# Performance work log

Hardware: AMD Instinct MI355X
Metric: run time of the kernel (lower is better)

Reference implementation:

```python
import jax, jax.numpy as jnp
import numpy as np

B, T, D = 2, 2048, 1024
H = 16
HD = D // H  # 64

def setup_inputs() -> dict:
    key = jax.random.key(0)
    k1, k2, k3 = jax.random.split(key, 3)
    x = jax.random.normal(k1, (B, T, D), dtype=jnp.float32)
    # Linear weights stored as [in, out] for x @ W (torch stores [out, in])
    W_qkv = jax.random.normal(k2, (D, 3 * D), dtype=jnp.float32) * (1.0 / np.sqrt(D))
    W_proj = jax.random.normal(k3, (D, D), dtype=jnp.float32) * (1.0 / np.sqrt(D))
    return {"x": x, "W_qkv": W_qkv, "W_proj": W_proj}

def reference(x, W_qkv, W_proj):
    Bx, Tx, C = x.shape
    qkv = x @ W_qkv                             # [B, T, 3D]
    q, k, v = jnp.split(qkv, 3, axis=-1)        # each [B, T, D]
    # [B, T, H, HD] -> [B, H, T, HD]
    q = q.reshape(Bx, Tx, H, HD).transpose(0, 2, 1, 3)
    k = k.reshape(Bx, Tx, H, HD).transpose(0, 2, 1, 3)
    v = v.reshape(Bx, Tx, H, HD).transpose(0, 2, 1, 3)
    scale = 1.0 / np.sqrt(HD).astype(np.float32)
    att = jnp.einsum('bhqd,bhkd->bhqk', q, k) * scale  # [B, H, T, T]
    causal = jnp.tril(jnp.ones((Tx, Tx), dtype=bool))
    att = jnp.where(causal[None, None, :, :], att, -jnp.inf)
    att = jax.nn.softmax(att, axis=-1)
    y = jnp.einsum('bhqk,bhkd->bhqd', att, v)   # [B, H, T, HD]
    y = y.transpose(0, 2, 1, 3).reshape(Bx, Tx, C)
    return y @ W_proj
```

## Files before the change

### kernel.cpp

```cpp
#include <hip/hip_runtime.h>

typedef __bf16 bf16x8 __attribute__((ext_vector_type(8)));
typedef __bf16 bf16x4 __attribute__((ext_vector_type(4)));
typedef float f32x4 __attribute__((ext_vector_type(4)));
typedef unsigned short u16;
typedef unsigned int u32;
typedef u32 u32x4 __attribute__((ext_vector_type(4)));

__device__ __forceinline__ u16 f2bf(float f) {
  u32 u = __builtin_bit_cast(u32, f);
  u += 0x7fffu + ((u >> 16) & 1u);
  return (u16)(u >> 16);
}

__device__ __forceinline__ u32 cvt_pk_bf16(float lo, float hi) {
  u32 r;
  asm("v_cvt_pk_bf16_f32 %0, %1, %2" : "=v"(r) : "v"(lo), "v"(hi));
  return r;
}

__device__ __forceinline__ float ex2(float x) {
  float r;
  asm("v_exp_f32 %0, %1" : "=v"(r) : "v"(x));
  return r;
}

__device__ __forceinline__ void gl_lds16(const u16* g, u16* l) {
  __builtin_amdgcn_global_load_lds(
      (const __attribute__((address_space(1))) u32*)g,
      (__attribute__((address_space(3))) u32*)l, 16, 0, 0);
}

__device__ __forceinline__ bf16x4 tr16(const u16* p) {
  bf16x4 r;
  auto lp = (const __attribute__((address_space(3))) u16*)p;
  asm volatile("ds_read_b64_tr_b16 %0, %1" : "=&v"(r) : "v"(lp));
  return r;
}

__global__ __launch_bounds__(256) void k_prep(const float* __restrict__ x,
                                              u16* __restrict__ Xb,
                                              const float* __restrict__ Wqkv,
                                              u16* __restrict__ Wqt,
                                              const float* __restrict__ Wproj,
                                              u16* __restrict__ Wpt) {
  __shared__ float tile[32][33];
  const int bid = blockIdx.x;
  if (bid < 2048) {
    int i = bid * 256 + threadIdx.x;
    const float4* p = (const float4*)x + (size_t)i * 2;
    float4 a = p[0], b = p[1];
    u16 r[8] = {f2bf(a.x), f2bf(a.y), f2bf(a.z), f2bf(a.w),
                f2bf(b.x), f2bf(b.y), f2bf(b.z), f2bf(b.w)};
    ((uint4*)Xb)[i] = *(const uint4*)r;
    return;
  }
  const float* in;
  u16* out;
  int K, N, n0, k0;
  if (bid < 5120) {
    in = Wqkv;
    out = Wqt;
    K = 1024;
    N = 3072;
    int idx = bid - 2048;
    n0 = (idx % 96) * 32;
    k0 = (idx / 96) * 32;
  } else {
    in = Wproj;
    out = Wpt;
    K = 1024;
    N = 1024;
    int idx = bid - 5120;
    n0 = (idx & 31) * 32;
    k0 = (idx >> 5) * 32;
  }
  int c = threadIdx.x & 31, r0 = (threadIdx.x >> 5) * 4;
#pragma unroll
  for (int rr = 0; rr < 4; ++rr) {
    int r = r0 + rr;
    tile[r][c] = in[(size_t)(k0 + r) * N + n0 + c];
  }
  __syncthreads();
#pragma unroll
  for (int rr = 0; rr < 4; ++rr) {
    int r = r0 + rr;
    out[(size_t)(n0 + r) * K + k0 + c] = f2bf(tile[c][r]);
  }
}

__global__ __launch_bounds__(256) void k_gemm0(const u16* __restrict__ A,
                                               const u16* __restrict__ Bt,
                                               u16* __restrict__ Qp, u16* __restrict__ Kp,
                                               u16* __restrict__ Vp, int K) {
  __shared__ char smem[128 * 136 * 2];
  u16* As = (u16*)smem;
  u16* Bs = (u16*)(smem + 16384);
  u16* Cs = (u16*)smem;
  const int tid = threadIdx.x;
  const int lane = tid & 63, wave = tid >> 6;
  const int l15 = lane & 15, l4 = lane >> 4;
  const int wr = wave >> 1, wc = wave & 1;
  const int tm = blockIdx.y, tn = blockIdx.x;

  int srow[4], scol[4];
#pragma unroll
  for (int i = 0; i < 4; ++i) {
    srow[i] = wave * 32 + i * 8 + (lane >> 3);
    scol[i] = ((lane & 7) ^ (srow[i] & 7)) * 8;
  }

  const f32x4 fz = {0.f, 0.f, 0.f, 0.f};
  f32x4 acc[4][4];
#pragma unroll
  for (int a = 0; a < 4; ++a)
#pragma unroll
    for (int b = 0; b < 4; ++b) acc[a][b] = fz;

  const int nk = K >> 6;
  for (int kt = 0; kt < nk; ++kt) {
#pragma unroll
    for (int i = 0; i < 4; ++i)
      gl_lds16(A + (size_t)(tm * 128 + srow[i]) * K + kt * 64 + scol[i],
               &As[(wave * 4 + i) * 512]);
#pragma unroll
    for (int i = 0; i < 4; ++i)
      gl_lds16(Bt + (size_t)(tn * 128 + srow[i]) * K + kt * 64 + scol[i],
               &Bs[(wave * 4 + i) * 512]);
    __syncthreads();
    bf16x8 af[2][4], bfr[2][4];
#pragma unroll
    for (int s = 0; s < 2; ++s) {
#pragma unroll
      for (int mi = 0; mi < 4; ++mi) {
        int row = wr * 64 + mi * 16 + l15;
        int pch = (s * 4 + l4) ^ (row & 7);
        af[s][mi] = *(const bf16x8*)&As[row * 64 + pch * 8];
      }
#pragma unroll
      for (int ni = 0; ni < 4; ++ni) {
        int row = wc * 64 + ni * 16 + l15;
        int pch = (s * 4 + l4) ^ (row & 7);
        bfr[s][ni] = *(const bf16x8*)&Bs[row * 64 + pch * 8];
      }
    }
    __builtin_amdgcn_s_setprio(1);
#pragma unroll
    for (int s = 0; s < 2; ++s)
#pragma unroll
      for (int mi = 0; mi < 4; ++mi)
#pragma unroll
        for (int ni = 0; ni < 4; ++ni)
          acc[mi][ni] = __builtin_amdgcn_mfma_f32_16x16x32_bf16(af[s][mi], bfr[s][ni],
                                                                acc[mi][ni], 0, 0, 0);
    __builtin_amdgcn_s_setprio(0);
    __syncthreads();
  }

#pragma unroll
  for (int ni = 0; ni < 4; ++ni) {
    int colb = wc * 64 + ni * 16;
    float scl = ((tn * 128 + colb) >> 10) == 0 ? 0.180336880f : 1.0f;
#pragma unroll
    for (int mi = 0; mi < 4; ++mi)
#pragma unroll
      for (int r = 0; r < 4; ++r) {
        int rowb = wr * 64 + mi * 16 + l4 * 4 + r;
        Cs[rowb * 136 + colb + l15] = f2bf(acc[mi][ni][r] * scl);
      }
  }
  __syncthreads();
#pragma unroll
  for (int pass = 0; pass < 8; ++pass) {
    int rowb = pass * 16 + (tid >> 4);
    int colb = (tid & 15) * 8;
    uint4 v = *(const uint4*)&Cs[rowb * 136 + colb];
    int rowg = tm * 128 + rowb;
    int b = rowg >> 11, t = rowg & 2047;
    int gcol = tn * 128 + colb;
    int which = gcol >> 10;
    int d = gcol & 1023;
    int h = d >> 6, hd = d & 63;
    u16* dst = which == 0 ? Qp : (which == 1 ? Kp : Vp);
    *(uint4*)&dst[(size_t)(((b * 16 + h) * 2048 + t) * 64 + hd)] = v;
  }
}

__global__ __launch_bounds__(256) void k_gemm1(const u16* __restrict__ A,
                                               const u16* __restrict__ Bt,
                                               float* __restrict__ Cf, int K) {
  __shared__ char smem1[128 * 68 * 4];
  u16* As = (u16*)smem1;
  u16* Bs = (u16*)(smem1 + 16384);
  float* Cs = (float*)smem1;
  const int tid = threadIdx.x;
  const int lane = tid & 63, wave = tid >> 6;
  const int l15 = lane & 15, l4 = lane >> 4;
  const int wr = wave >> 1, wc = wave & 1;
  const int tm = blockIdx.y, tn = blockIdx.x;

  int srowA[4], scolA[4], srowB[2], scolB[2];
#pragma unroll
  for (int i = 0; i < 4; ++i) {
    srowA[i] = wave * 32 + i * 8 + (lane >> 3);
    scolA[i] = ((lane & 7) ^ (srowA[i] & 7)) * 8;
  }
#pragma unroll
  for (int i = 0; i < 2; ++i) {
    srowB[i] = wave * 16 + i * 8 + (lane >> 3);
    scolB[i] = ((lane & 7) ^ (srowB[i] & 7)) * 8;
  }

  const f32x4 fz = {0.f, 0.f, 0.f, 0.f};
  f32x4 acc[4][2];
#pragma unroll
  for (int a = 0; a < 4; ++a)
#pragma unroll
    for (int b = 0; b < 2; ++b) acc[a][b] = fz;

  const int nk = K >> 6;
  for (int kt = 0; kt < nk; ++kt) {
#pragma unroll
    for (int i = 0; i < 4; ++i)
      gl_lds16(A + (size_t)(tm * 128 + srowA[i]) * K + kt * 64 + scolA[i],
               &As[(wave * 4 + i) * 512]);
#pragma unroll
    for (int i = 0; i < 2; ++i)
      gl_lds16(Bt + (size_t)(tn * 64 + srowB[i]) * K + kt * 64 + scolB[i],
               &Bs[(wave * 2 + i) * 512]);
    __syncthreads();
    bf16x8 af[2][4], bfr[2][2];
#pragma unroll
    for (int s = 0; s < 2; ++s) {
#pragma unroll
      for (int mi = 0; mi < 4; ++mi) {
        int row = wr * 64 + mi * 16 + l15;
        int pch = (s * 4 + l4) ^ (row & 7);
        af[s][mi] = *(const bf16x8*)&As[row * 64 + pch * 8];
      }
#pragma unroll
      for (int ni = 0; ni < 2; ++ni) {
        int row = wc * 32 + ni * 16 + l15;
        int pch = (s * 4 + l4) ^ (row & 7);
        bfr[s][ni] = *(const bf16x8*)&Bs[row * 64 + pch * 8];
      }
    }
    __builtin_amdgcn_s_setprio(1);
#pragma unroll
    for (int s = 0; s < 2; ++s)
#pragma unroll
      for (int mi = 0; mi < 4; ++mi)
#pragma unroll
        for (int ni = 0; ni < 2; ++ni)
          acc[mi][ni] = __builtin_amdgcn_mfma_f32_16x16x32_bf16(af[s][mi], bfr[s][ni],
                                                                acc[mi][ni], 0, 0, 0);
    __builtin_amdgcn_s_setprio(0);
    __syncthreads();
  }

#pragma unroll
  for (int mi = 0; mi < 4; ++mi)
#pragma unroll
    for (int ni = 0; ni < 2; ++ni)
#pragma unroll
      for (int r = 0; r < 4; ++r) {
        int rowb = wr * 64 + mi * 16 + l4 * 4 + r;
        Cs[rowb * 68 + wc * 32 + ni * 16 + l15] = acc[mi][ni][r];
      }
  __syncthreads();
#pragma unroll
  for (int pass = 0; pass < 8; ++pass) {
    int rowb = pass * 16 + (tid >> 4);
    int colb = (tid & 15) * 4;
    float4 v = *(const float4*)&Cs[rowb * 68 + colb];
    *(float4*)&Cf[(size_t)(tm * 128 + rowb) * 1024 + tn * 64 + colb] = v;
  }
}

__global__ __launch_bounds__(256) void k_attn(const u16* __restrict__ Q,
                                              const u16* __restrict__ K,
                                              const u16* __restrict__ V,
                                              u16* __restrict__ Y) {
  __shared__ u16 Kl[4][64 * 64];
  __shared__ u16 Vtr[4][64 * 64];
  const int tid = threadIdx.x, lane = tid & 63, wave = tid >> 6;
  const int l15 = lane & 15, l4 = lane >> 4;
  const int L = blockIdx.y * 16 + blockIdx.x;
  const int g = L & 7, j = L >> 3;
  const int bh = (g << 2) + (j >> 4);
  const int pp = j & 15;
  const int qtA = 31 - pp, qtB = pp;
  const u16* Qb = Q + (size_t)bh * 2048 * 64;
  const u16* Kb = K + (size_t)bh * 2048 * 64;
  const u16* Vb = V + (size_t)bh * 2048 * 64;
  const int b = bh >> 4, h = bh & 15;
  const f32x4 fz = {0.f, 0.f, 0.f, 0.f};

  const int kk0 = wave * 16 + (lane >> 3);
  const int kk1 = kk0 + 8;
  const int lcol0 = ((lane & 7) ^ (kk0 & 7)) * 8;
  const int lcol1 = ((lane & 7) ^ (kk1 & 7)) * 8;
  int vk[2], vhd[2];
#pragma unroll
  for (int i = 0; i < 2; ++i) {
    int o = (wave * 2 + i) * 512 + lane * 8;
    vk[i] = ((o >> 6) & 15) * 4 + ((o >> 4) & 3);
    vhd[i] = ((o >> 10) << 4) + (o & 8);
  }

  auto stage = [&](int buf, int kt) {
    gl_lds16(Kb + (size_t)(kt * 64 + kk0) * 64 + lcol0, &Kl[buf][(wave * 2 + 0) * 512]);
    gl_lds16(Kb + (size_t)(kt * 64 + kk1) * 64 + lcol1, &Kl[buf][(wave * 2 + 1) * 512]);
    gl_lds16(Vb + (size_t)(kt * 64 + vk[0]) * 64 + vhd[0], &Vtr[buf][(wave * 2 + 0) * 512]);
    gl_lds16(Vb + (size_t)(kt * 64 + vk[1]) * 64 + vhd[1], &Vtr[buf][(wave * 2 + 1) * 512]);
  };

  auto qk = [&](int buf, const bf16x8* qf, f32x4* accS) {
#pragma unroll
    for (int s = 0; s < 2; ++s)
#pragma unroll
      for (int nb = 0; nb < 4; ++nb) {
        int kk = nb * 16 + l15;
        int ch = (s * 4 + l4) ^ (kk & 7);
        bf16x8 kf = *(const bf16x8*)&Kl[buf][kk * 64 + ch * 8];
        accS[nb] = __builtin_amdgcn_mfma_f32_16x16x32_bf16(kf, qf[s], accS[nb], 0, 0, 0);
      }
  };
  auto pv = [&](int buf, const bf16x8* pf, f32x4* accO) {
    bf16x8 vf[2][4];
#pragma unroll
    for (int s = 0; s < 2; ++s)
#pragma unroll
      for (int hb = 0; hb < 4; ++hb) {
        bf16x4 ta = tr16(&Vtr[buf][(hb * 16 + s * 8) * 64 + lane * 4]);
        bf16x4 tb = tr16(&Vtr[buf][(hb * 16 + s * 8 + 4) * 64 + lane * 4]);
        vf[s][hb] = __builtin_shufflevector(ta, tb, 0, 1, 2, 3, 4, 5, 6, 7);
      }
    asm volatile("s_waitcnt lgkmcnt(0)" ::: "memory");
    __builtin_amdgcn_sched_barrier(0);
    __builtin_amdgcn_s_setprio(1);
#pragma unroll
    for (int s = 0; s < 2; ++s)
#pragma unroll
      for (int hb = 0; hb < 4; ++hb)
        accO[hb] = __builtin_amdgcn_mfma_f32_16x16x32_bf16(vf[s][hb], pf[s], accO[hb], 0, 0, 0);
    __builtin_amdgcn_s_setprio(0);
  };

  bf16x8 qfA[2], qfB[2];
  {
    int qrA = qtA * 64 + wave * 16 + l15;
    int qrB = qtB * 64 + wave * 16 + l15;
    qfA[0] = *(const bf16x8*)&Qb[(size_t)qrA * 64 + l4 * 8];
    qfA[1] = *(const bf16x8*)&Qb[(size_t)qrA * 64 + 32 + l4 * 8];
    qfB[0] = *(const bf16x8*)&Qb[(size_t)qrB * 64 + l4 * 8];
    qfB[1] = *(const bf16x8*)&Qb[(size_t)qrB * 64 + 32 + l4 * 8];
  }
  f32x4 oA[4] = {fz, fz, fz, fz}, oB[4] = {fz, fz, fz, fz};
  float mA = -1e30f, lsA = 0.f, mB = -1e30f, lsB = 0.f;

  stage(0, 0);
  stage(1, 1);
  stage(2, 2);
  int cur = 0;
#pragma unroll 1
  for (int kt = 0; kt <= qtB; ++kt) {
    asm volatile("s_waitcnt vmcnt(8)" ::: "memory");
    __builtin_amdgcn_s_barrier();
    __builtin_amdgcn_sched_barrier(0);

    f32x4 sA[4] = {fz, fz, fz, fz}, sB[4] = {fz, fz, fz, fz};
    __builtin_amdgcn_s_setprio(1);
#pragma unroll
    for (int s = 0; s < 2; ++s)
#pragma unroll
      for (int nb = 0; nb < 4; ++nb) {
        int kk = nb * 16 + l15;
        int ch = (s * 4 + l4) ^ (kk & 7);
        bf16x8 kf = *(const bf16x8*)&Kl[cur][kk * 64 + ch * 8];
        sA[nb] = __builtin_amdgcn_mfma_f32_16x16x32_bf16(kf, qfA[s], sA[nb], 0, 0, 0);
        sB[nb] = __builtin_amdgcn_mfma_f32_16x16x32_bf16(kf, qfB[s], sB[nb], 0, 0, 0);
      }
    __builtin_amdgcn_s_setprio(0);

    float vA[16], vB[16];
#pragma unroll
    for (int nb = 0; nb < 4; ++nb)
#pragma unroll
      for (int r = 0; r < 4; ++r) {
        vA[nb * 4 + r] = sA[nb][r];
        vB[nb * 4 + r] = sB[nb][r];
      }
    if (kt == qtB) {
      int qg = wave * 16 + l15;
#pragma unroll
      for (int i = 0; i < 16; ++i) {
        int kg = (i >> 2) * 16 + l4 * 4 + (i & 3);
        if (kg > qg) vB[i] = -1e30f;
      }
    }
    float tA[8], tB[8];
#pragma unroll
    for (int i = 0; i < 8; ++i) {
      tA[i] = fmaxf(vA[2 * i], vA[2 * i + 1]);
      tB[i] = fmaxf(vB[2 * i], vB[2 * i + 1]);
    }
#pragma unroll
    for (int i = 0; i < 4; ++i) {
      tA[i] = fmaxf(tA[i], tA[i + 4]);
      tB[i] = fmaxf(tB[i], tB[i + 4]);
    }
    float mxA = fmaxf(fmaxf(tA[0], tA[2]), fmaxf(tA[1], tA[3]));
    float mxB = fmaxf(fmaxf(tB[0], tB[2]), fmaxf(tB[1], tB[3]));
    if (!__all(fmaxf(mxA - mA, mxB - mB) <= 8.0f)) {
      float mrA = fmaxf(mxA, __shfl_xor(mxA, 16));
      float mrB = fmaxf(mxB, __shfl_xor(mxB, 16));
      mrA = fmaxf(mrA, __shfl_xor(mrA, 32));
      mrB = fmaxf(mrB, __shfl_xor(mrB, 32));
      float mnA = fmaxf(mA, mrA), mnB = fmaxf(mB, mrB);
      float aA = ex2(mA - mnA), aB = ex2(mB - mnB);
      mA = mnA;
      mB = mnB;
      lsA *= aA;
      lsB *= aB;
#pragma unroll
      for (int hb = 0; hb < 4; ++hb)
#pragma unroll
        for (int r = 0; r < 4; ++r) {
          oA[hb][r] *= aA;
          oB[hb][r] *= aB;
        }
    }
    float pA[16], pB[16];
#pragma unroll
    for (int i = 0; i < 16; ++i) {
      pA[i] = ex2(vA[i] - mA);
      pB[i] = ex2(vB[i] - mB);
    }
    float uA[8], uB[8];
#pragma unroll
    for (int i = 0; i < 8; ++i) {
      uA[i] = pA[2 * i] + pA[2 * i + 1];
      uB[i] = pB[2 * i] + pB[2 * i + 1];
    }
#pragma unroll
    for (int i = 0; i < 4; ++i) {
      uA[i] += uA[i + 4];
      uB[i] += uB[i + 4];
    }
    lsA += (uA[0] + uA[2]) + (uA[1] + uA[3]);
    lsB += (uB[0] + uB[2]) + (uB[1] + uB[3]);
    bf16x8 pfA[2], pfB[2];
#pragma unroll
    for (int s = 0; s < 2; ++s) {
      u32x4 wa, wb;
      wa.x = cvt_pk_bf16(pA[8 * s + 0], pA[8 * s + 1]);
      wb.x = cvt_pk_bf16(pB[8 * s + 0], pB[8 * s + 1]);
      wa.y = cvt_pk_bf16(pA[8 * s + 2], pA[8 * s + 3]);
      wb.y = cvt_pk_bf16(pB[8 * s + 2], pB[8 * s + 3]);
      wa.z = cvt_pk_bf16(pA[8 * s + 4], pA[8 * s + 5]);
      wb.z = cvt_pk_bf16(pB[8 * s + 4], pB[8 * s + 5]);
      wa.w = cvt_pk_bf16(pA[8 * s + 6], pA[8 * s + 7]);
      wb.w = cvt_pk_bf16(pB[8 * s + 6], pB[8 * s + 7]);
      pfA[s] = __builtin_bit_cast(bf16x8, wa);
      pfB[s] = __builtin_bit_cast(bf16x8, wb);
    }
    {
      bf16x8 vf[2][4];
#pragma unroll
      for (int s = 0; s < 2; ++s)
#pragma unroll
        for (int hb = 0; hb < 4; ++hb) {
          bf16x4 ta = tr16(&Vtr[cur][(hb * 16 + s * 8) * 64 + lane * 4]);
          bf16x4 tb = tr16(&Vtr[cur][(hb * 16 + s * 8 + 4) * 64 + lane * 4]);
          vf[s][hb] = __builtin_shufflevector(ta, tb, 0, 1, 2, 3, 4, 5, 6, 7);
        }
      asm volatile("s_waitcnt lgkmcnt(0)" ::: "memory");
      __builtin_amdgcn_sched_barrier(0);
      __builtin_amdgcn_s_setprio(1);
#pragma unroll
      for (int s = 0; s < 2; ++s)
#pragma unroll
        for (int hb = 0; hb < 4; ++hb) {
          oA[hb] = __builtin_amdgcn_mfma_f32_16x16x32_bf16(vf[s][hb], pfA[s], oA[hb], 0, 0, 0);
          oB[hb] = __builtin_amdgcn_mfma_f32_16x16x32_bf16(vf[s][hb], pfB[s], oB[hb], 0, 0, 0);
        }
      __builtin_amdgcn_s_setprio(0);
    }

    int nt = kt + 3 > qtB ? qtB : kt + 3;
    stage((cur + 3) & 3, nt);
    cur = (cur + 1) & 3;
  }

  const int t0 = qtB + 1;
  const int rem = qtA - qtB;
  const int nd = (rem - 1) >> 1;
  __builtin_amdgcn_s_barrier();
  __builtin_amdgcn_sched_barrier(0);
#pragma unroll
  for (int i = 0; i < 4; ++i) {
    int tt = t0 + i > qtA ? qtA : t0 + i;
    stage(i, tt);
  }

  auto smx2 = [&](f32x4* s1, f32x4* s2, bf16x8* pf1, bf16x8* pf2) {
    float v1[16], v2[16];
#pragma unroll
    for (int nb = 0; nb < 4; ++nb)
#pragma unroll
      for (int r = 0; r < 4; ++r) {
        v1[nb * 4 + r] = s1[nb][r];
        v2[nb * 4 + r] = s2[nb][r];
      }
    float t1[8], t2[8];
#pragma unroll
    for (int i = 0; i < 8; ++i) {
      t1[i] = fmaxf(v1[2 * i], v1[2 * i + 1]);
      t2[i] = fmaxf(v2[2 * i], v2[2 * i + 1]);
    }
#pragma unroll
    for (int i = 0; i < 4; ++i) {
      t1[i] = fmaxf(t1[i], t1[i + 4]);
      t2[i] = fmaxf(t2[i], t2[i + 4]);
    }
    float mx = fmaxf(fmaxf(fmaxf(t1[0], t1[2]), fmaxf(t1[1], t1[3])),
                     fmaxf(fmaxf(t2[0], t2[2]), fmaxf(t2[1], t2[3])));
    if (!__all(mx <= mA + 8.0f)) {
      float mr = fmaxf(mx, __shfl_xor(mx, 16));
      mr = fmaxf(mr, __shfl_xor(mr, 32));
      float mn = fmaxf(mA, mr);
      float a = ex2(mA - mn);
      mA = mn;
      lsA *= a;
#pragma unroll
      for (int hb = 0; hb < 4; ++hb)
#pragma unroll
        for (int r = 0; r < 4; ++r) oA[hb][r] *= a;
    }
    float p1[16], p2[16];
#pragma unroll
    for (int i = 0; i < 16; ++i) {
      p1[i] = ex2(v1[i] - mA);
      p2[i] = ex2(v2[i] - mA);
    }
    float u1[8], u2[8];
#pragma unroll
    for (int i = 0; i < 8; ++i) {
      u1[i] = p1[2 * i] + p1[2 * i + 1];
      u2[i] = p2[2 * i] + p2[2 * i + 1];
    }
#pragma unroll
    for (int i = 0; i < 4; ++i) {
      u1[i] += u1[i + 4];
      u2[i] += u2[i + 4];
    }
    lsA += (u1[0] + u1[2]) + (u1[1] + u1[3]) + (u2[0] + u2[2]) + (u2[1] + u2[3]);
#pragma unroll
    for (int s = 0; s < 2; ++s) {
      u32x4 w1, w2;
      w1.x = cvt_pk_bf16(p1[8 * s + 0], p1[8 * s + 1]);
      w2.x = cvt_pk_bf16(p2[8 * s + 0], p2[8 * s + 1]);
      w1.y = cvt_pk_bf16(p1[8 * s + 2], p1[8 * s + 3]);
      w2.y = cvt_pk_bf16(p2[8 * s + 2], p2[8 * s + 3]);
      w1.z = cvt_pk_bf16(p1[8 * s + 4], p1[8 * s + 5]);
      w2.z = cvt_pk_bf16(p2[8 * s + 4], p2[8 * s + 5]);
      w1.w = cvt_pk_bf16(p1[8 * s + 6], p1[8 * s + 7]);
      w2.w = cvt_pk_bf16(p2[8 * s + 6], p2[8 * s + 7]);
      pf1[s] = __builtin_bit_cast(bf16x8, w1);
      pf2[s] = __builtin_bit_cast(bf16x8, w2);
    }
  };

#pragma unroll 1
  for (int j2 = 0; j2 < nd; ++j2) {
    asm volatile("s_waitcnt vmcnt(8)" ::: "memory");
    __builtin_amdgcn_s_barrier();
    __builtin_amdgcn_sched_barrier(0);
    int b0 = (2 * j2) & 3, b1 = (2 * j2 + 1) & 3;

    f32x4 s1[4] = {fz, fz, fz, fz}, s2[4] = {fz, fz, fz, fz};
    __builtin_amdgcn_s_setprio(1);
    qk(b0, qfA, s1);
    qk(b1, qfA, s2);
    __builtin_amdgcn_s_setprio(0);
    bf16x8 pf1[2], pf2[2];
    smx2(s1, s2, pf1, pf2);
    pv(b0, pf1, oA);
    pv(b1, pf2, oA);

    __builtin_amdgcn_s_barrier();
    __builtin_amdgcn_sched_barrier(0);
    int ta = t0 + 2 * j2 + 4, tb2 = t0 + 2 * j2 + 5;
    stage(b0, ta > qtA ? qtA : ta);
    stage(b1, tb2 > qtA ? qtA : tb2);
  }

  {
    asm volatile("s_waitcnt vmcnt(8)" ::: "memory");
    __builtin_amdgcn_s_barrier();
    __builtin_amdgcn_sched_barrier(0);
    int buf = (rem - 1) & 3;
    f32x4 sA[4] = {fz, fz, fz, fz};
    __builtin_amdgcn_s_setprio(1);
    qk(buf, qfA, sA);
    __builtin_amdgcn_s_setprio(0);
    float vA[16];
#pragma unroll
    for (int nb = 0; nb < 4; ++nb)
#pragma unroll
      for (int r = 0; r < 4; ++r) vA[nb * 4 + r] = sA[nb][r];
    int qg = wave * 16 + l15;
#pragma unroll
    for (int i = 0; i < 16; ++i) {
      int kg = (i >> 2) * 16 + l4 * 4 + (i & 3);
      if (kg > qg) vA[i] = -1e30f;
    }
    float tA[8];
#pragma unroll
    for (int i = 0; i < 8; ++i) tA[i] = fmaxf(vA[2 * i], vA[2 * i + 1]);
#pragma unroll
    for (int i = 0; i < 4; ++i) tA[i] = fmaxf(tA[i], tA[i + 4]);
    float mxA = fmaxf(fmaxf(tA[0], tA[2]), fmaxf(tA[1], tA[3]));
    if (!__all(mxA <= mA + 8.0f)) {
      float mrA = fmaxf(mxA, __shfl_xor(mxA, 16));
      mrA = fmaxf(mrA, __shfl_xor(mrA, 32));
      float mnA = fmaxf(mA, mrA);
      float aA = ex2(mA - mnA);
      mA = mnA;
      lsA *= aA;
#pragma unroll
      for (int hb = 0; hb < 4; ++hb)
#pragma unroll
        for (int r = 0; r < 4; ++r) oA[hb][r] *= aA;
    }
    float pA[16];
#pragma unroll
    for (int i = 0; i < 16; ++i) pA[i] = ex2(vA[i] - mA);
    float uA[8];
#pragma unroll
    for (int i = 0; i < 8; ++i) uA[i] = pA[2 * i] + pA[2 * i + 1];
#pragma unroll
    for (int i = 0; i < 4; ++i) uA[i] += uA[i + 4];
    lsA += (uA[0] + uA[2]) + (uA[1] + uA[3]);
    bf16x8 pfA[2];
#pragma unroll
    for (int s = 0; s < 2; ++s) {
      u32x4 wa;
      wa.x = cvt_pk_bf16(pA[8 * s + 0], pA[8 * s + 1]);
      wa.y = cvt_pk_bf16(pA[8 * s + 2], pA[8 * s + 3]);
      wa.z = cvt_pk_bf16(pA[8 * s + 4], pA[8 * s + 5]);
      wa.w = cvt_pk_bf16(pA[8 * s + 6], pA[8 * s + 7]);
      pfA[s] = __builtin_bit_cast(bf16x8, wa);
    }
    pv(buf, pfA, oA);
  }

  auto epi = [&](f32x4* accO, float lsum, int qt) {
    float t = lsum + __shfl_xor(lsum, 16);
    t += __shfl_xor(t, 32);
    float inv = 1.0f / t;
    int qg = qt * 64 + wave * 16 + l15;
    u16* yrow = Y + (size_t)(b * 2048 + qg) * 1024 + h * 64;
#pragma unroll
    for (int hb = 0; hb < 4; ++hb) {
      uint2 pk;
      pk.x = cvt_pk_bf16(accO[hb][0] * inv, accO[hb][1] * inv);
      pk.y = cvt_pk_bf16(accO[hb][2] * inv, accO[hb][3] * inv);
      *(uint2*)&yrow[hb * 16 + l4 * 4] = pk;
    }
  };
  epi(oA, lsA, qtA);
  epi(oB, lsB, qtB);
}

extern "C" void kernel_launch(void* const* d_in, const int* in_sizes, int n_in,
                              void* d_out, int out_size, void* d_ws, size_t ws_size,
                              hipStream_t stream) {
  const float* x = (const float*)d_in[0];
  const float* Wqkv = (const float*)d_in[1];
  const float* Wproj = (const float*)d_in[2];
  float* out = (float*)d_out;

  char* ws = (char*)d_ws;
  u16* Xb  = (u16*)(ws + 0);
  u16* Wqt = (u16*)(ws + ((size_t)8 << 20));
  u16* Wpt = (u16*)(ws + ((size_t)14 << 20));
  u16* Qs  = (u16*)(ws + ((size_t)16 << 20));
  u16* Ks  = (u16*)(ws + ((size_t)24 << 20));
  u16* Vs  = (u16*)(ws + ((size_t)32 << 20));
  u16* Yb  = (u16*)(ws + ((size_t)40 << 20));

  k_prep<<<6144, 256, 0, stream>>>(x, Xb, Wqkv, Wqt, Wproj, Wpt);
  k_gemm0<<<dim3(24, 32), 256, 0, stream>>>(Xb, Wqt, Qs, Ks, Vs, 1024);
  k_attn<<<dim3(16, 32), 256, 0, stream>>>(Qs, Ks, Vs, Yb);
  k_gemm1<<<dim3(16, 32), 256, 0, stream>>>(Yb, Wpt, out, 1024);
}
```

Measured before the change: 91.47 us.

## Restructure KV tile pipeline into batched stage/consume rounds with vmcnt(0) waits

Replaces the per-tile 4-buffer rolling prefetch (vmcnt(8) waits, one stage per iteration) and the paired-tile A-only loop with a generic scheme. Each round consumes up to 2 (AB phase) or 4 (A-only phase) staged tiles, then refills buffers up to four ahead. The A-only loop drops the fused two-tile softmax and applies the causal mask only on the diagonal tile. The cost is full vmcnt(0) drains per round, which reduce load/compute overlap compared with the prior rolling pipeline.

```diff
diff --git a/kernel.cpp b/kernel.cpp
--- a/kernel.cpp
+++ b/kernel.cpp
@@ -359,16 +359,8 @@
   f32x4 oA[4] = {fz, fz, fz, fz}, oB[4] = {fz, fz, fz, fz};
   float mA = -1e30f, lsA = 0.f, mB = -1e30f, lsB = 0.f;
 
-  stage(0, 0);
-  stage(1, 1);
-  stage(2, 2);
-  int cur = 0;
-#pragma unroll 1
-  for (int kt = 0; kt <= qtB; ++kt) {
-    asm volatile("s_waitcnt vmcnt(8)" ::: "memory");
-    __builtin_amdgcn_s_barrier();
-    __builtin_amdgcn_sched_barrier(0);
-
+  auto bodyAB = [&](int kt) {
+    const int buf = kt & 3;
     f32x4 sA[4] = {fz, fz, fz, fz}, sB[4] = {fz, fz, fz, fz};
     __builtin_amdgcn_s_setprio(1);
 #pragma unroll
@@ -377,7 +369,7 @@
       for (int nb = 0; nb < 4; ++nb) {
         int kk = nb * 16 + l15;
         int ch = (s * 4 + l4) ^ (kk & 7);
-        bf16x8 kf = *(const bf16x8*)&Kl[cur][kk * 64 + ch * 8];
+        bf16x8 kf = *(const bf16x8*)&Kl[buf][kk * 64 + ch * 8];
         sA[nb] = __builtin_amdgcn_mfma_f32_16x16x32_bf16(kf, qfA[s], sA[nb], 0, 0, 0);
         sB[nb] = __builtin_amdgcn_mfma_f32_16x16x32_bf16(kf, qfB[s], sB[nb], 0, 0, 0);
       }
@@ -465,142 +457,30 @@
       pfA[s] = __builtin_bit_cast(bf16x8, wa);
       pfB[s] = __builtin_bit_cast(bf16x8, wb);
     }
-    {
-      bf16x8 vf[2][4];
-#pragma unroll
-      for (int s = 0; s < 2; ++s)
-#pragma unroll
-        for (int hb = 0; hb < 4; ++hb) {
-          bf16x4 ta = tr16(&Vtr[cur][(hb * 16 + s * 8) * 64 + lane * 4]);
-          bf16x4 tb = tr16(&Vtr[cur][(hb * 16 + s * 8 + 4) * 64 + lane * 4]);
-          vf[s][hb] = __builtin_shufflevector(ta, tb, 0, 1, 2, 3, 4, 5, 6, 7);
-        }
-      asm volatile("s_waitcnt lgkmcnt(0)" ::: "memory");
-      __builtin_amdgcn_sched_barrier(0);
-      __builtin_amdgcn_s_setprio(1);
-#pragma unroll
-      for (int s = 0; s < 2; ++s)
-#pragma unroll
-        for (int hb = 0; hb < 4; ++hb) {
-          oA[hb] = __builtin_amdgcn_mfma_f32_16x16x32_bf16(vf[s][hb], pfA[s], oA[hb], 0, 0, 0);
-          oB[hb] = __builtin_amdgcn_mfma_f32_16x16x32_bf16(vf[s][hb], pfB[s], oB[hb], 0, 0, 0);
-        }
-      __builtin_amdgcn_s_setprio(0);
-    }
-
-    int nt = kt + 3 > qtB ? qtB : kt + 3;
-    stage((cur + 3) & 3, nt);
-    cur = (cur + 1) & 3;
-  }
-
-  const int t0 = qtB + 1;
-  const int rem = qtA - qtB;
-  const int nd = (rem - 1) >> 1;
-  __builtin_amdgcn_s_barrier();
-  __builtin_amdgcn_sched_barrier(0);
-#pragma unroll
-  for (int i = 0; i < 4; ++i) {
-    int tt = t0 + i > qtA ? qtA : t0 + i;
-    stage(i, tt);
-  }
-
-  auto smx2 = [&](f32x4* s1, f32x4* s2, bf16x8* pf1, bf16x8* pf2) {
-    float v1[16], v2[16];
-#pragma unroll
-    for (int nb = 0; nb < 4; ++nb)
-#pragma unroll
-      for (int r = 0; r < 4; ++r) {
-        v1[nb * 4 + r] = s1[nb][r];
-        v2[nb * 4 + r] = s2[nb][r];
-      }
-    float t1[8], t2[8];
-#pragma unroll
-    for (int i = 0; i < 8; ++i) {
-      t1[i] = fmaxf(v1[2 * i], v1[2 * i + 1]);
-      t2[i] = fmaxf(v2[2 * i], v2[2 * i + 1]);
-    }
-#pragma unroll
-    for (int i = 0; i < 4; ++i) {
-      t1[i] = fmaxf(t1[i], t1[i + 4]);
-      t2[i] = fmaxf(t2[i], t2[i + 4]);
-    }
-    float mx = fmaxf(fmaxf(fmaxf(t1[0], t1[2]), fmaxf(t1[1], t1[3])),
-                     fmaxf(fmaxf(t2[0], t2[2]), fmaxf(t2[1], t2[3])));
-    if (!__all(mx <= mA + 8.0f)) {
-      float mr = fmaxf(mx, __shfl_xor(mx, 16));
-      mr = fmaxf(mr, __shfl_xor(mr, 32));
-      float mn = fmaxf(mA, mr);
-      float a = ex2(mA - mn);
-      mA = mn;
-      lsA *= a;
-#pragma unroll
-      for (int hb = 0; hb < 4; ++hb)
-#pragma unroll
-        for (int r = 0; r < 4; ++r) oA[hb][r] *= a;
-    }
-    float p1[16], p2[16];
-#pragma unroll
-    for (int i = 0; i < 16; ++i) {
-      p1[i] = ex2(v1[i] - mA);
-      p2[i] = ex2(v2[i] - mA);
-    }
-    float u1[8], u2[8];
-#pragma unroll
-    for (int i = 0; i < 8; ++i) {
-      u1[i] = p1[2 * i] + p1[2 * i + 1];
-      u2[i] = p2[2 * i] + p2[2 * i + 1];
-    }
-#pragma unroll
-    for (int i = 0; i < 4; ++i) {
-      u1[i] += u1[i + 4];
-      u2[i] += u2[i + 4];
-    }
-    lsA += (u1[0] + u1[2]) + (u1[1] + u1[3]) + (u2[0] + u2[2]) + (u2[1] + u2[3]);
-#pragma unroll
-    for (int s = 0; s < 2; ++s) {
-      u32x4 w1, w2;
-      w1.x = cvt_pk_bf16(p1[8 * s + 0], p1[8 * s + 1]);
-      w2.x = cvt_pk_bf16(p2[8 * s + 0], p2[8 * s + 1]);
-      w1.y = cvt_pk_bf16(p1[8 * s + 2], p1[8 * s + 3]);
-      w2.y = cvt_pk_bf16(p2[8 * s + 2], p2[8 * s + 3]);
-      w1.z = cvt_pk_bf16(p1[8 * s + 4], p1[8 * s + 5]);
-      w2.z = cvt_pk_bf16(p2[8 * s + 4], p2[8 * s + 5]);
-      w1.w = cvt_pk_bf16(p1[8 * s + 6], p1[8 * s + 7]);
-      w2.w = cvt_pk_bf16(p2[8 * s + 6], p2[8 * s + 7]);
-      pf1[s] = __builtin_bit_cast(bf16x8, w1);
-      pf2[s] = __builtin_bit_cast(bf16x8, w2);
-    }
+    bf16x8 vf[2][4];
+#pragma unroll
+    for (int s = 0; s < 2; ++s)
+#pragma unroll
+      for (int hb = 0; hb < 4; ++hb) {
+        bf16x4 ta = tr16(&Vtr[buf][(hb * 16 + s * 8) * 64 + lane * 4]);
+        bf16x4 tb = tr16(&Vtr[buf][(hb * 16 + s * 8 + 4) * 64 + lane * 4]);
+        vf[s][hb] = __builtin_shufflevector(ta, tb, 0, 1, 2, 3, 4, 5, 6, 7);
+      }
+    asm volatile("s_waitcnt lgkmcnt(0)" ::: "memory");
+    __builtin_amdgcn_sched_barrier(0);
+    __builtin_amdgcn_s_setprio(1);
+#pragma unroll
+    for (int s = 0; s < 2; ++s)
+#pragma unroll
+      for (int hb = 0; hb < 4; ++hb) {
+        oA[hb] = __builtin_amdgcn_mfma_f32_16x16x32_bf16(vf[s][hb], pfA[s], oA[hb], 0, 0, 0);
+        oB[hb] = __builtin_amdgcn_mfma_f32_16x16x32_bf16(vf[s][hb], pfB[s], oB[hb], 0, 0, 0);
+      }
+    __builtin_amdgcn_s_setprio(0);
   };
 
-#pragma unroll 1
-  for (int j2 = 0; j2 < nd; ++j2) {
-    asm volatile("s_waitcnt vmcnt(8)" ::: "memory");
-    __builtin_amdgcn_s_barrier();
-    __builtin_amdgcn_sched_barrier(0);
-    int b0 = (2 * j2) & 3, b1 = (2 * j2 + 1) & 3;
-
-    f32x4 s1[4] = {fz, fz, fz, fz}, s2[4] = {fz, fz, fz, fz};
-    __builtin_amdgcn_s_setprio(1);
-    qk(b0, qfA, s1);
-    qk(b1, qfA, s2);
-    __builtin_amdgcn_s_setprio(0);
-    bf16x8 pf1[2], pf2[2];
-    smx2(s1, s2, pf1, pf2);
-    pv(b0, pf1, oA);
-    pv(b1, pf2, oA);
-
-    __builtin_amdgcn_s_barrier();
-    __builtin_amdgcn_sched_barrier(0);
-    int ta = t0 + 2 * j2 + 4, tb2 = t0 + 2 * j2 + 5;
-    stage(b0, ta > qtA ? qtA : ta);
-    stage(b1, tb2 > qtA ? qtA : tb2);
-  }
-
-  {
-    asm volatile("s_waitcnt vmcnt(8)" ::: "memory");
-    __builtin_amdgcn_s_barrier();
-    __builtin_amdgcn_sched_barrier(0);
-    int buf = (rem - 1) & 3;
+  auto bodyA = [&](int kt) {
+    const int buf = kt & 3;
     f32x4 sA[4] = {fz, fz, fz, fz};
     __builtin_amdgcn_s_setprio(1);
     qk(buf, qfA, sA);
@@ -610,11 +490,13 @@
     for (int nb = 0; nb < 4; ++nb)
 #pragma unroll
       for (int r = 0; r < 4; ++r) vA[nb * 4 + r] = sA[nb][r];
-    int qg = wave * 16 + l15;
-#pragma unroll
-    for (int i = 0; i < 16; ++i) {
-      int kg = (i >> 2) * 16 + l4 * 4 + (i & 3);
-      if (kg > qg) vA[i] = -1e30f;
+    if (kt == qtA) {
+      int qg = wave * 16 + l15;
+#pragma unroll
+      for (int i = 0; i < 16; ++i) {
+        int kg = (i >> 2) * 16 + l4 * 4 + (i & 3);
+        if (kg > qg) vA[i] = -1e30f;
+      }
     }
     float tA[8];
 #pragma unroll
@@ -654,6 +536,47 @@
       pfA[s] = __builtin_bit_cast(bf16x8, wa);
     }
     pv(buf, pfA, oA);
+  };
+
+#pragma unroll
+  for (int t = 0; t < 4; ++t) stage(t, t);
+  int stageNext = 4;
+  int consumed = 0;
+
+#pragma unroll 1
+  while (consumed <= qtB) {
+    int end = consumed + 2 <= qtB + 1 ? consumed + 2 : qtB + 1;
+    asm volatile("s_waitcnt vmcnt(0)" ::: "memory");
+    __builtin_amdgcn_s_barrier();
+    __builtin_amdgcn_sched_barrier(0);
+#pragma unroll 1
+    for (int kt = consumed; kt < end; ++kt) bodyAB(kt);
+    __builtin_amdgcn_s_barrier();
+    __builtin_amdgcn_sched_barrier(0);
+    consumed = end;
+#pragma unroll 1
+    while (stageNext < consumed + 4 && stageNext <= qtA) {
+      stage(stageNext & 3, stageNext);
+      ++stageNext;
+    }
+  }
+
+#pragma unroll 1
+  while (consumed <= qtA) {
+    int end = consumed + 4 <= qtA + 1 ? consumed + 4 : qtA + 1;
+    asm volatile("s_waitcnt vmcnt(0)" ::: "memory");
+    __builtin_amdgcn_s_barrier();
+    __builtin_amdgcn_sched_barrier(0);
+#pragma unroll 1
+    for (int kt = consumed; kt < end; ++kt) bodyA(kt);
+    __builtin_amdgcn_s_barrier();
+    __builtin_amdgcn_sched_barrier(0);
+    consumed = end;
+#pragma unroll 1
+    while (stageNext < consumed + 4 && stageNext <= qtA) {
+      stage(stageNext & 3, stageNext);
+      ++stageNext;
+    }
   }
 
   auto epi = [&](f32x4* accO, float lsum, int qt) {
```

Result: slower. 94.76 us (+3.6%).
